# Kernel optimization log

Measured on AMD Instinct MI355X. Metric: run time of the kernel, lower is better.

Reference implementation:

```python
import jax, jax.numpy as jnp
import numpy as np

# Dimensions: B jets, P max particles, C coords, F features, K neighbors,
# H hidden units, O MLP output dim. Edge feature dim E = 2*(C+F).
B, P, C, F, K, H, O = 256, 128, 2, 7, 16, 128, 256
E = 2 * (C + F)
BIG = 1e9  # distance assigned to invalid (padded) neighbors


def setup_inputs() -> dict:
    key = jax.random.key(0)
    k1, k2, k3, k4 = jax.random.split(key, 4)
    raw = jax.random.normal(k1, (B, P, C + F), dtype=jnp.float32)
    # per-jet particle counts in [K+2, P]; padding is contiguous at the end
    lengths = jax.random.randint(k2, (B,), K + 2, P + 1)
    mask = (jnp.arange(P)[None, :] < lengths[:, None]).astype(jnp.float32)  # [B,P]
    # zero out padded rows and append mask as the last column (as the layer expects)
    x = jnp.concatenate([raw * mask[..., None], mask[..., None]], axis=-1)  # [B,P,C+F+1]
    W1 = jax.random.normal(k3, (E, H), dtype=jnp.float32) * (1.0 / np.sqrt(E))
    b1 = jnp.zeros((H,), dtype=jnp.float32)
    W2 = jax.random.normal(k4, (H, O), dtype=jnp.float32) * (1.0 / np.sqrt(H))
    b2 = jnp.zeros((O,), dtype=jnp.float32)
    return {"x": x, "W1": W1, "b1": b1, "W2": W2, "b2": b2}


def reference(x, W1, b1, W2, b2):
    coords = x[..., :C]          # [B,P,C]
    feats = x[..., C:-1]         # [B,P,F]
    mask = x[..., -1]            # [B,P] 1=real particle, 0=padding
    valid = mask > 0

    # --- kNN on coordinates (masked, vectorized over jets) ---
    diff = coords[:, :, None, :] - coords[:, None, :, :]      # [B,P,P,C]
    # squared distance: same ordering as tf.norm, avoids sqrt-at-zero issues
    dist2 = jnp.sum(diff * diff, axis=-1)                      # [B,P,P]
    dist2 = jnp.where(valid[:, None, :], dist2, BIG)           # mask padded neighbors
    _, idx = jax.lax.top_k(-dist2, K + 1)                      # [B,P,K+1]
    idx = idx[..., 1:]                                         # drop self -> [B,P,K]

    # --- gather neighbor coords/features ---
    idx_flat = idx.reshape(B, P * K)
    nbr_c = jnp.take_along_axis(coords, idx_flat[..., None], axis=1).reshape(B, P, K, C)
    nbr_f = jnp.take_along_axis(feats, idx_flat[..., None], axis=1).reshape(B, P, K, F)
    ctr_c = jnp.broadcast_to(coords[:, :, None, :], (B, P, K, C))
    ctr_f = jnp.broadcast_to(feats[:, :, None, :], (B, P, K, F))

    # edge features: [coord_i, feat_i, coord_j - coord_i, feat_j - feat_i]
    edge = jnp.concatenate([ctr_c, ctr_f, nbr_c - ctr_c, nbr_f - ctr_f], axis=-1)  # [B,P,K,E]

    # --- MLP + mean aggregation over neighbors ---
    h = jax.nn.relu(edge @ W1 + b1)   # [B,P,K,H]
    h = jax.nn.relu(h @ W2 + b2)      # [B,P,K,O]
    avg = jnp.mean(h, axis=2)         # [B,P,O]

    # append mask column; zero out padded particles (matches _fix_number_of_particles)
    out = jnp.concatenate([avg, jnp.ones((B, P, 1), avg.dtype)], axis=-1) * mask[..., None]
    return out
```

## Files before the change

### kernel.cpp

```cpp
#include <hip/hip_runtime.h>

#define BB 256
#define PP 128
#define KK 16
#define HH 128
#define OO 256
#define EE 18
#define XCH 10
#define BIGD 1000000000.0f
#define GPT 4

typedef __bf16 bf16x8 __attribute__((ext_vector_type(8)));
typedef __bf16 bf16x4 __attribute__((ext_vector_type(4)));
typedef float  f32x4  __attribute__((ext_vector_type(4)));

__global__ __launch_bounds__(256) void pack_w_kernel(const float* __restrict__ W1,
                                                     const float* __restrict__ W2,
                                                     __bf16* __restrict__ W2p,
                                                     __bf16* __restrict__ W1p) {
    const int t = blockIdx.x * 256 + threadIdx.x;
    if (t < 32768) {
        const int j  = t & 7;
        const int l  = (t >> 3) & 63;
        const int ks = (t >> 9) & 3;
        const int ct = t >> 11;
        const int row = ks * 32 + ((l >> 4) * 8) + j;
        const int col = ct * 16 + (l & 15);
        W2p[t] = (__bf16)W2[row * OO + col];
    } else {
        const int t2 = t - 32768;
        const int j  = t2 & 7;
        const int l  = (t2 >> 3) & 63;
        const int nt = t2 >> 9;
        const int k  = ((l >> 4) * 8) + j;
        const int n  = nt * 16 + (l & 15);
        W1p[t2] = (k < EE) ? (__bf16)W1[k * HH + n] : (__bf16)0.0f;
    }
}

__global__ __launch_bounds__(256, 4) void mlp_kernel(const float* __restrict__ x,
                                                     const __bf16* __restrict__ W1p,
                                                     const float* __restrict__ b1,
                                                     const __bf16* __restrict__ W2p,
                                                     const float* __restrict__ b2,
                                                     float* __restrict__ out) {
    __shared__ __bf16 sh1A[16 * 64 * 8];
    __shared__ float  sb1[HH];
    __shared__ float  sb2[OO];
    __shared__ float  smask[GPT];
    __shared__ int    sknn[GPT][KK];

    const int tid = threadIdx.x;
    const int lane = tid & 63;
    const int w = tid >> 6;
    const int quad = lane >> 4;
    const int lcol = lane & 15;

    const int pbase = blockIdx.x * GPT;
    const int bidx = pbase >> 7;
    const int i0 = pbase & (PP - 1);
    const float* xb = x + (size_t)bidx * PP * XCH;
    float* outrow = out + (size_t)pbase * (OO + 1);

    if (tid < HH) sb1[tid] = b1[tid];
    sb2[tid] = b2[tid];
    if (tid < GPT) smask[tid] = xb[(i0 + tid) * XCH + (XCH - 1)];
    __syncthreads();

    const bool allmasked =
        (smask[0] == 0.0f) & (smask[1] == 0.0f) & (smask[2] == 0.0f) & (smask[3] == 0.0f);
    if (allmasked) {
        for (int o = tid; o < GPT * (OO + 1); o += 256) outrow[o] = 0.0f;
        return;
    }

    const int i = i0 + w;
    if (smask[w] != 0.0f) {
        const float cix = xb[i * XCH + 0];
        const float ciy = xb[i * XCH + 1];

        const int j0 = lane, j1 = lane + 64;
        float d0, d1;
        {
            const float2 c0 = *(const float2*)(xb + j0 * XCH);
            const float m0 = xb[j0 * XCH + (XCH - 1)];
            float dx = cix - c0.x, dy = ciy - c0.y;
            d0 = __fadd_rn(__fmul_rn(dx, dx), __fmul_rn(dy, dy));
            if (m0 <= 0.0f || j0 == i) d0 = BIGD;
        }
        {
            const float2 c1 = *(const float2*)(xb + j1 * XCH);
            const float m1 = xb[j1 * XCH + (XCH - 1)];
            float dx = cix - c1.x, dy = ciy - c1.y;
            d1 = __fadd_rn(__fmul_rn(dx, dx), __fmul_rn(dy, dy));
            if (m1 <= 0.0f || j1 == i) d1 = BIGD;
        }

        const unsigned d0b = __float_as_uint(d0);
        const unsigned d1b = __float_as_uint(d1);

        unsigned long long A0 = ~0ull, A1 = ~0ull, W0 = 0ull, W1 = 0ull;
        int need = KK;
        int asz = 2 * 64;

        auto step = [&](unsigned long long q0, unsigned long long q1) {
            const unsigned long long z0 = A0 & q0;
            const unsigned long long z1 = A1 & q1;
            const int c = __popcll(z0) + __popcll(z1);
            if (c == need) { W0 |= z0; W1 |= z1; A0 = A1 = 0ull; need = 0; }
            else if (c > need) { A0 = z0; A1 = z1; asz = c; }
            else { W0 |= z0; W1 |= z1; need -= c; A0 &= ~z0; A1 &= ~z1; asz -= c; }
        };

#pragma unroll 1
        for (int t = 14; t >= 0; --t) {
            const unsigned dg0 = (d0b >> (2 * t + 1)) & 3u;
            const unsigned dg1 = (d1b >> (2 * t + 1)) & 3u;
            const unsigned long long p0_0  = __ballot(dg0 == 0u);
            const unsigned long long p1_0  = __ballot(dg1 == 0u);
            const unsigned long long p0_01 = __ballot(dg0 <= 1u);
            const unsigned long long p1_01 = __ballot(dg1 <= 1u);
            const unsigned long long p0_02 = __ballot(dg0 <= 2u);
            const unsigned long long p1_02 = __ballot(dg1 <= 2u);
            const unsigned long long z0_0  = A0 & p0_0,  z1_0  = A1 & p1_0;
            const unsigned long long z0_01 = A0 & p0_01, z1_01 = A1 & p1_01;
            const unsigned long long z0_02 = A0 & p0_02, z1_02 = A1 & p1_02;
            const int c0  = __popcll(z0_0)  + __popcll(z1_0);
            const int c01 = __popcll(z0_01) + __popcll(z1_01);
            const int c02 = __popcll(z0_02) + __popcll(z1_02);
            if (c0 >= need) {
                A0 = z0_0; A1 = z1_0; asz = c0;
            } else if (c01 >= need) {
                W0 |= z0_0; W1 |= z1_0; need -= c0;
                A0 = z0_01 & ~p0_0; A1 = z1_01 & ~p1_0; asz = c01 - c0;
            } else if (c02 >= need) {
                W0 |= z0_01; W1 |= z1_01; need -= c01;
                A0 = z0_02 & ~p0_01; A1 = z1_02 & ~p1_01; asz = c02 - c01;
            } else {
                W0 |= z0_02; W1 |= z1_02; need -= c02;
                A0 &= ~p0_02; A1 &= ~p1_02; asz -= c02;
            }
            if (asz == need) { W0 |= A0; W1 |= A1; A0 = A1 = 0ull; need = 0; break; }
        }
        if (need) {
            const unsigned long long q0 = __ballot((d0b & 1u) == 0u);
            const unsigned long long q1 = __ballot((d1b & 1u) == 0u);
            step(q0, q1);
        }
        if (need) step(~0ull, 0ull);
        {
            const unsigned long long M5 = 0x00000000FFFFFFFFull;
            const unsigned long long M4 = 0x0000FFFF0000FFFFull;
            const unsigned long long M3 = 0x00FF00FF00FF00FFull;
            const unsigned long long M2 = 0x0F0F0F0F0F0F0F0Full;
            const unsigned long long M1 = 0x3333333333333333ull;
            const unsigned long long M0 = 0x5555555555555555ull;
            if (need) step(M5, M5);
            if (need) step(M4, M4);
            if (need) step(M3, M3);
            if (need) step(M2, M2);
            if (need) step(M1, M1);
            if (need) step(M0, M0);
        }
        W0 |= A0; W1 |= A1;

        unsigned int mb0 = __builtin_amdgcn_mbcnt_lo((unsigned)(W0 & 0xffffffffull), 0u);
        mb0 = __builtin_amdgcn_mbcnt_hi((unsigned)(W0 >> 32), mb0);
        unsigned int mb1 = __builtin_amdgcn_mbcnt_lo((unsigned)(W1 & 0xffffffffull), 0u);
        mb1 = __builtin_amdgcn_mbcnt_hi((unsigned)(W1 >> 32), mb1);
        const int base1 = __popcll(W0);

        if ((W0 >> lane) & 1ull) sknn[w][mb0] = j0;
        if ((W1 >> lane) & 1ull) sknn[w][base1 + mb1] = j1;
    } else {
        if (lane < KK) sknn[w][lane] = 0;
    }

    const int jn = sknn[w][lcol];
    const float* ci = xb + i * XCH;
    const float* cj = xb + jn * XCH;
    const float2 a01 = *(const float2*)(ci + 0);
    const float2 a23 = *(const float2*)(ci + 2);
    const float2 a45 = *(const float2*)(ci + 4);
    const float2 a67 = *(const float2*)(ci + 6);
    const float  a8  = ci[8];
    const float2 n01 = *(const float2*)(cj + 0);
    const float2 n23 = *(const float2*)(cj + 2);
    const float2 n45 = *(const float2*)(cj + 4);
    const float2 n67 = *(const float2*)(cj + 6);
    const float  n8  = cj[8];

    float v[8];
#pragma unroll
    for (int e = 0; e < 8; ++e) v[e] = 0.0f;
    if (quad == 0) {
        v[0] = a01.x; v[1] = a01.y; v[2] = a23.x; v[3] = a23.y;
        v[4] = a45.x; v[5] = a45.y; v[6] = a67.x; v[7] = a67.y;
    } else if (quad == 1) {
        v[0] = a8;
        v[1] = n01.x - a01.x; v[2] = n01.y - a01.y;
        v[3] = n23.x - a23.x; v[4] = n23.y - a23.y;
        v[5] = n45.x - a45.x; v[6] = n45.y - a45.y;
        v[7] = n67.x - a67.x;
    } else if (quad == 2) {
        v[0] = n67.y - a67.y;
        v[1] = n8 - a8;
    }

    bf16x8 ef;
#pragma unroll
    for (int e = 0; e < 8; ++e) ef[e] = (__bf16)v[e];

    bf16x8 wf[8];
#pragma unroll
    for (int nt = 0; nt < 8; ++nt)
        wf[nt] = *(const bf16x8*)&W1p[(size_t)((nt * 64 + lane) * 8)];

    const f32x4 z4 = {0.0f, 0.0f, 0.0f, 0.0f};
    f32x4 h[8];
#pragma unroll
    for (int nt = 0; nt < 8; ++nt)
        h[nt] = __builtin_amdgcn_mfma_f32_16x16x32_bf16(wf[nt], ef, z4, 0, 0, 0);

#pragma unroll
    for (int nt = 0; nt < 8; ++nt) {
        const int ks = nt >> 1;
        const int lp = (((nt * 2 + (quad >> 1)) & 3) << 4) | lcol;
        bf16x4 hv;
#pragma unroll
        for (int r = 0; r < 4; ++r) {
            const int m = nt * 16 + quad * 4 + r;
            hv[r] = (__bf16)fmaxf(h[nt][r] + sb1[m], 0.0f);
        }
        *(bf16x4*)&sh1A[((ks * GPT + w) * 64 + lp) * 8 + (quad & 1) * 4] = hv;
    }
    __syncthreads();

    f32x4 acc[GPT][4];
#pragma unroll
    for (int g = 0; g < GPT; ++g)
#pragma unroll
        for (int ct = 0; ct < 4; ++ct) acc[g][ct] = z4;

#pragma unroll
    for (int ks = 0; ks < 4; ++ks) {
        bf16x8 af[GPT], bfr[4];
#pragma unroll
        for (int g = 0; g < GPT; ++g)
            af[g] = *(const bf16x8*)&sh1A[((ks * GPT + g) * 64 + lane) * 8];
#pragma unroll
        for (int ct = 0; ct < 4; ++ct)
            bfr[ct] = *(const bf16x8*)&W2p[(size_t)((((w * 4 + ct) * 4 + ks) * 64 + lane) * 8)];
#pragma unroll
        for (int g = 0; g < GPT; ++g)
#pragma unroll
            for (int ct = 0; ct < 4; ++ct)
                acc[g][ct] = __builtin_amdgcn_mfma_f32_16x16x32_bf16(
                    af[g], bfr[ct], acc[g][ct], 0, 0, 0);
    }

    float val[4];
#pragma unroll
    for (int g = 0; g < GPT; ++g) {
#pragma unroll
        for (int ct = 0; ct < 4; ++ct) {
            const int col = w * 64 + ct * 16 + lcol;
            const float bc = sb2[col];
            float s = 0.0f;
#pragma unroll
            for (int r = 0; r < 4; ++r) s += fmaxf(acc[g][ct][r] + bc, 0.0f);
            s += __shfl_xor(s, 16, 64);
            s += __shfl_xor(s, 32, 64);
            if (quad == g) val[ct] = s;
        }
    }
    const float m = smask[quad] * (1.0f / KK);
#pragma unroll
    for (int ct = 0; ct < 4; ++ct)
        outrow[(size_t)quad * (OO + 1) + w * 64 + ct * 16 + lcol] = val[ct] * m;
    if (tid < GPT) outrow[(size_t)tid * (OO + 1) + OO] = smask[tid];
}

extern "C" void kernel_launch(void* const* d_in, const int* in_sizes, int n_in,
                              void* d_out, int out_size, void* d_ws, size_t ws_size,
                              hipStream_t stream) {
    const float* x  = (const float*)d_in[0];
    const float* W1 = (const float*)d_in[1];
    const float* b1 = (const float*)d_in[2];
    const float* W2 = (const float*)d_in[3];
    const float* b2 = (const float*)d_in[4];
    float* out = (float*)d_out;

    __bf16* W2p = (__bf16*)d_ws;
    __bf16* W1p = (__bf16*)((char*)d_ws + 65536);

    pack_w_kernel<<<144, 256, 0, stream>>>(W1, W2, W2p, W1p);

    const int nblocks = (BB * PP) / GPT;
    mlp_kernel<<<nblocks, 256, 0, stream>>>(x, W1p, b1, W2p, b2, out);
}
```

Before: 128.6 us.

## Drop shared bias/mask staging, hoist W1 loads, split second GEMM into column chunks

```diff
diff --git a/kernel.cpp b/kernel.cpp
--- a/kernel.cpp
+++ b/kernel.cpp
@@ -45,9 +45,6 @@
                                                      const float* __restrict__ b2,
                                                      float* __restrict__ out) {
     __shared__ __bf16 sh1A[16 * 64 * 8];
-    __shared__ float  sb1[HH];
-    __shared__ float  sb2[OO];
-    __shared__ float  smask[GPT];
     __shared__ int    sknn[GPT][KK];
 
     const int tid = threadIdx.x;
@@ -62,22 +59,30 @@
     const float* xb = x + (size_t)bidx * PP * XCH;
     float* outrow = out + (size_t)pbase * (OO + 1);
 
-    if (tid < HH) sb1[tid] = b1[tid];
-    sb2[tid] = b2[tid];
-    if (tid < GPT) smask[tid] = xb[(i0 + tid) * XCH + (XCH - 1)];
-    __syncthreads();
-
-    const bool allmasked =
-        (smask[0] == 0.0f) & (smask[1] == 0.0f) & (smask[2] == 0.0f) & (smask[3] == 0.0f);
-    if (allmasked) {
+    const float mq = xb[(i0 + quad) * XCH + (XCH - 1)];
+    const int i = i0 + w;
+
+    if (__all(mq == 0.0f)) {
         for (int o = tid; o < GPT * (OO + 1); o += 256) outrow[o] = 0.0f;
         return;
     }
 
-    const int i = i0 + w;
-    if (smask[w] != 0.0f) {
-        const float cix = xb[i * XCH + 0];
-        const float ciy = xb[i * XCH + 1];
+    bf16x8 wf[8];
+#pragma unroll
+    for (int nt = 0; nt < 8; ++nt)
+        wf[nt] = *(const bf16x8*)&W1p[(size_t)((nt * 64 + lane) * 8)];
+
+    const float* ci = xb + i * XCH;
+    const float2 a01 = *(const float2*)(ci + 0);
+    const float2 a23 = *(const float2*)(ci + 2);
+    const float2 a45 = *(const float2*)(ci + 4);
+    const float2 a67 = *(const float2*)(ci + 6);
+    const float  a8  = ci[8];
+    const float  mw  = ci[XCH - 1];
+
+    if (mw != 0.0f) {
+        const float cix = a01.x;
+        const float ciy = a01.y;
 
         const int j0 = lane, j1 = lane + 64;
         float d0, d1;
@@ -177,13 +182,7 @@
     }
 
     const int jn = sknn[w][lcol];
-    const float* ci = xb + i * XCH;
     const float* cj = xb + jn * XCH;
-    const float2 a01 = *(const float2*)(ci + 0);
-    const float2 a23 = *(const float2*)(ci + 2);
-    const float2 a45 = *(const float2*)(ci + 4);
-    const float2 a67 = *(const float2*)(ci + 6);
-    const float  a8  = ci[8];
     const float2 n01 = *(const float2*)(cj + 0);
     const float2 n23 = *(const float2*)(cj + 2);
     const float2 n45 = *(const float2*)(cj + 4);
@@ -211,11 +210,6 @@
 #pragma unroll
     for (int e = 0; e < 8; ++e) ef[e] = (__bf16)v[e];
 
-    bf16x8 wf[8];
-#pragma unroll
-    for (int nt = 0; nt < 8; ++nt)
-        wf[nt] = *(const bf16x8*)&W1p[(size_t)((nt * 64 + lane) * 8)];
-
     const f32x4 z4 = {0.0f, 0.0f, 0.0f, 0.0f};
     f32x4 h[8];
 #pragma unroll
@@ -226,59 +220,60 @@
     for (int nt = 0; nt < 8; ++nt) {
         const int ks = nt >> 1;
         const int lp = (((nt * 2 + (quad >> 1)) & 3) << 4) | lcol;
+        const f32x4 b1v = *(const f32x4*)&b1[nt * 16 + quad * 4];
         bf16x4 hv;
 #pragma unroll
-        for (int r = 0; r < 4; ++r) {
-            const int m = nt * 16 + quad * 4 + r;
-            hv[r] = (__bf16)fmaxf(h[nt][r] + sb1[m], 0.0f);
-        }
+        for (int r = 0; r < 4; ++r)
+            hv[r] = (__bf16)fmaxf(h[nt][r] + b1v[r], 0.0f);
         *(bf16x4*)&sh1A[((ks * GPT + w) * 64 + lp) * 8 + (quad & 1) * 4] = hv;
     }
     __syncthreads();
 
-    f32x4 acc[GPT][4];
-#pragma unroll
-    for (int g = 0; g < GPT; ++g)
-#pragma unroll
-        for (int ct = 0; ct < 4; ++ct) acc[g][ct] = z4;
-
-#pragma unroll
-    for (int ks = 0; ks < 4; ++ks) {
-        bf16x8 af[GPT], bfr[4];
-#pragma unroll
-        for (int g = 0; g < GPT; ++g)
-            af[g] = *(const bf16x8*)&sh1A[((ks * GPT + g) * 64 + lane) * 8];
-#pragma unroll
-        for (int ct = 0; ct < 4; ++ct)
-            bfr[ct] = *(const bf16x8*)&W2p[(size_t)((((w * 4 + ct) * 4 + ks) * 64 + lane) * 8)];
-#pragma unroll
-        for (int g = 0; g < GPT; ++g)
-#pragma unroll
-            for (int ct = 0; ct < 4; ++ct)
-                acc[g][ct] = __builtin_amdgcn_mfma_f32_16x16x32_bf16(
-                    af[g], bfr[ct], acc[g][ct], 0, 0, 0);
-    }
-
-    float val[4];
-#pragma unroll
-    for (int g = 0; g < GPT; ++g) {
-#pragma unroll
-        for (int ct = 0; ct < 4; ++ct) {
+    const float mscale = mq * (1.0f / KK);
+#pragma unroll
+    for (int ch = 0; ch < 2; ++ch) {
+        f32x4 acc[GPT][2];
+#pragma unroll
+        for (int g = 0; g < GPT; ++g) { acc[g][0] = z4; acc[g][1] = z4; }
+
+#pragma unroll
+        for (int ks = 0; ks < 4; ++ks) {
+            bf16x8 af[GPT], bfr[2];
+#pragma unroll
+            for (int g = 0; g < GPT; ++g)
+                af[g] = *(const bf16x8*)&sh1A[((ks * GPT + g) * 64 + lane) * 8];
+#pragma unroll
+            for (int c = 0; c < 2; ++c) {
+                const int ct = ch * 2 + c;
+                bfr[c] = *(const bf16x8*)&W2p[(size_t)((((w * 4 + ct) * 4 + ks) * 64 + lane) * 8)];
+            }
+#pragma unroll
+            for (int g = 0; g < GPT; ++g)
+#pragma unroll
+                for (int c = 0; c < 2; ++c)
+                    acc[g][c] = __builtin_amdgcn_mfma_f32_16x16x32_bf16(
+                        af[g], bfr[c], acc[g][c], 0, 0, 0);
+        }
+
+#pragma unroll
+        for (int c = 0; c < 2; ++c) {
+            const int ct = ch * 2 + c;
             const int col = w * 64 + ct * 16 + lcol;
-            const float bc = sb2[col];
-            float s = 0.0f;
-#pragma unroll
-            for (int r = 0; r < 4; ++r) s += fmaxf(acc[g][ct][r] + bc, 0.0f);
-            s += __shfl_xor(s, 16, 64);
-            s += __shfl_xor(s, 32, 64);
-            if (quad == g) val[ct] = s;
-        }
-    }
-    const float m = smask[quad] * (1.0f / KK);
-#pragma unroll
-    for (int ct = 0; ct < 4; ++ct)
-        outrow[(size_t)quad * (OO + 1) + w * 64 + ct * 16 + lcol] = val[ct] * m;
-    if (tid < GPT) outrow[(size_t)tid * (OO + 1) + OO] = smask[tid];
+            const float bc = b2[col];
+            float val = 0.0f;
+#pragma unroll
+            for (int g = 0; g < GPT; ++g) {
+                float s = 0.0f;
+#pragma unroll
+                for (int r = 0; r < 4; ++r) s += fmaxf(acc[g][c][r] + bc, 0.0f);
+                s += __shfl_xor(s, 16, 64);
+                s += __shfl_xor(s, 32, 64);
+                if (quad == g) val = s;
+            }
+            outrow[(size_t)quad * (OO + 1) + col] = val * mscale;
+        }
+    }
+    if (tid < GPT) outrow[(size_t)tid * (OO + 1) + OO] = xb[(i0 + tid) * XCH + (XCH - 1)];
 }
 
 extern "C" void kernel_launch(void* const* d_in, const int* in_sizes, int n_in,
```

Result: faster. 125.6 us (-2.3%).
